# Kernel optimization log

Measured on AMD Instinct MI355X. Metric: run time of the kernel, lower is better.

Reference implementation:

```python
import jax, jax.numpy as jnp
import numpy as np

EPS = 1e-12
NUM_ITERATIONS = 3


def squash(t, axis=-1):
    sn = jnp.sum(t * t, axis=axis, keepdims=True)
    scale = sn / (1.0 + sn + EPS)
    return scale * t / jnp.sqrt(sn + EPS)


def setup_inputs() -> dict:
    key = jax.random.key(0)
    k1, k2 = jax.random.split(key)
    B, R, IN, OUT, C = 128, 4096, 16, 32, 2
    x = jax.random.normal(k1, (B, R, IN), dtype=jnp.float32)
    # learned parameter: torch.randn(num_capsules, num_route_nodes, in, out)
    route_weights = jax.random.normal(k2, (C, R, IN, OUT), dtype=jnp.float32)
    return {"x": x, "route_weights": route_weights}


def reference(x, route_weights):
    # priors: [C, B, R, 1, O] == x[None,:,:,None,:] @ W[:,None,:,:,:]
    priors = jnp.einsum('bri,crio->cbro', x, route_weights)[..., None, :]
    # logits kept [C,B,R,1,1]: the torch code stores [C,B,R,1,O] but every
    # update (delta_logits) is constant along O, so softmax over axis=2 is identical.
    logits = jnp.zeros(priors.shape[:-1] + (1,), dtype=priors.dtype)
    outputs = None
    for i in range(NUM_ITERATIONS):
        probs = jax.nn.softmax(logits, axis=2)                      # over route nodes
        s = jnp.sum(probs * priors, axis=2, keepdims=True)          # [C,B,1,1,O]
        outputs = squash(s, axis=-1)
        if i != NUM_ITERATIONS - 1:
            delta = jnp.sum(priors * outputs, axis=-1, keepdims=True)  # [C,B,R,1,1]
            logits = logits + delta
    return outputs
```

## Files before the change

### kernel.cpp

```cpp
#include <hip/hip_runtime.h>
#include <hip/hip_cooperative_groups.h>
#include <math.h>

namespace cg = cooperative_groups;

#define CB    128
#define CR    4096
#define CIN   16
#define COUT  32
#define CCAP  2
#define RC    16
#define NRCH  (CR / RC)
#define GRID  (CCAP * NRCH)
#define EPSF  1e-12f

typedef _Float16 h8  __attribute__((ext_vector_type(8)));
typedef _Float16 h4t __attribute__((ext_vector_type(4)));
typedef float    f4  __attribute__((ext_vector_type(4)));

__device__ __forceinline__ void stage_pack_W(const float* __restrict__ w,
                                             int c, int r0, int t,
                                             _Float16* WpL, float* Stg)
{
  h4t* WpL4 = (h4t*)WpL;
#pragma unroll
  for (int h = 0; h < 2; ++h) {
    const float4* src = (const float4*)(w + ((size_t)c * CR + r0 + h * 8) * 512);
    ((float4*)Stg)[t]       = src[t];
    ((float4*)Stg)[t + 512] = src[t + 512];
    __syncthreads();
#pragma unroll
    for (int q = 0; q < 2; ++q) {
      const int sl  = t * 2 + q;
      const int rr  = sl >> 7;
      const int rem = sl & 127;
      const int ot  = rem >> 6;
      const int gs  = (rem >> 4) & 3;
      const int ms  = rem & 15;
      h4t v;
#pragma unroll
      for (int j = 0; j < 4; ++j)
        v[j] = (_Float16)Stg[rr * 512 + (4 * gs + j) * 32 + ot * 16 + ms];
      WpL4[(h * 8 + rr) * 128 + rem] = v;
    }
    __syncthreads();
  }
}

__device__ __forceinline__ void pass_body(const float* __restrict__ x,
                                          const float* __restrict__ vsum,
                                          float* __restrict__ partialA,
                                          float* __restrict__ partialE,
                                          const _Float16* WpL,
                                          int c, int rch, int t, int uniform)
{
  const int r0 = rch * RC;
  const int wv = t >> 6, L = t & 63, g = L >> 4, m = L & 15;
  const int b  = wv * 16 + m;
  const h4t* WpL4 = (const h4t*)WpL;

  float4 vA = {0.f, 0.f, 0.f, 0.f}, vB = {0.f, 0.f, 0.f, 0.f};
  if (!uniform) {
    const float* vb = vsum + ((size_t)c * CB + b) * COUT;
    vA = *(const float4*)(vb + 4 * g);
    vB = *(const float4*)(vb + 16 + 4 * g);
  }
  float accA[4] = {0.f, 0.f, 0.f, 0.f};
  float accB[4] = {0.f, 0.f, 0.f, 0.f};
  float esum = 0.f;

#pragma unroll 4
  for (int ri = 0; ri < RC; ++ri) {
    const int r = r0 + ri;
    float4 xf = *(const float4*)(x + ((size_t)b * CR + r) * CIN + 4 * g);
    h8 bx = {(_Float16)xf.x, (_Float16)xf.y, (_Float16)xf.z, (_Float16)xf.w,
             (_Float16)0.f, (_Float16)0.f, (_Float16)0.f, (_Float16)0.f};
    h4t wA4 = WpL4[ri * 128 + L];
    h4t wB4 = WpL4[ri * 128 + 64 + L];
    h8 aA = {wA4[0], wA4[1], wA4[2], wA4[3],
             (_Float16)0.f, (_Float16)0.f, (_Float16)0.f, (_Float16)0.f};
    h8 aB = {wB4[0], wB4[1], wB4[2], wB4[3],
             (_Float16)0.f, (_Float16)0.f, (_Float16)0.f, (_Float16)0.f};
    f4 z = {0.f, 0.f, 0.f, 0.f};
    f4 pA = __builtin_amdgcn_mfma_f32_16x16x32_f16(aA, bx, z, 0, 0, 0);
    f4 pB = __builtin_amdgcn_mfma_f32_16x16x32_f16(aB, bx, z, 0, 0, 0);

    float e = 1.f;
    if (!uniform) {
      float d = pA[0] * vA.x + pA[1] * vA.y + pA[2] * vA.z + pA[3] * vA.w
              + pB[0] * vB.x + pB[1] * vB.y + pB[2] * vB.z + pB[3] * vB.w;
      d += __shfl_xor(d, 16);
      d += __shfl_xor(d, 32);
      e = __expf(d);
    }
    esum += e;
#pragma unroll
    for (int j = 0; j < 4; ++j) { accA[j] += e * pA[j]; accB[j] += e * pB[j]; }
  }

  float4 a4 = {accA[0], accA[1], accA[2], accA[3]};
  float4 b4 = {accB[0], accB[1], accB[2], accB[3]};
  float* dst = partialA + ((size_t)(c * NRCH + rch)) * 4096 + (size_t)t * 8;
  *(float4*)dst = a4;
  *(float4*)(dst + 4) = b4;
  if (g == 0) partialE[((size_t)(c * NRCH + rch)) * CB + b] = esum;
}

template <int JG>
__device__ __forceinline__ void redv_body(const float* __restrict__ partialA,
                                          const float* __restrict__ partialE,
                                          float* __restrict__ vsum,
                                          float* __restrict__ out,
                                          float (*red)[33], float* rede,
                                          int cb, int t, int mode)
{
  const int c2 = cb >> 7, b2 = cb & 127;
  const int o = t & 31, jg = t >> 5;
  const int wv2 = b2 >> 4, m2 = b2 & 15;
  const int half = o >> 4, oo = o & 15, g2 = oo >> 2, j2 = oo & 3;
  const size_t idx = (size_t)(wv2 * 64 + g2 * 16 + m2) * 8 + half * 4 + j2;

  float s = 0.f;
#pragma unroll 4
  for (int k = 0; k < NRCH / JG; ++k) {
    const int j = jg + k * JG;
    s += partialA[((size_t)(c2 * NRCH + j)) * 4096 + idx];
  }
  red[jg][o] = s;
  __syncthreads();

  if (t < JG) {
    float e = 0.f;
#pragma unroll 4
    for (int k = 0; k < NRCH / JG; ++k)
      e += partialE[((size_t)(c2 * NRCH + t + k * JG)) * CB + b2];
    rede[t] = e;
  }
  __syncthreads();

  if (t < 32) {
    float sv = 0.f, es = 0.f;
#pragma unroll
    for (int jj = 0; jj < JG; ++jj) { sv += red[jj][t]; es += rede[jj]; }
    float sm = sv / es;
    float sn = sm * sm;
#pragma unroll
    for (int sh = 1; sh < 32; sh <<= 1) sn += __shfl_xor(sn, sh);
    float fac = sn / ((1.f + sn + EPSF) * sqrtf(sn + EPSF));
    float vv = sm * fac;
    if (mode == 2)      out[cb * COUT + t]  = vv;
    else if (mode == 1) vsum[cb * COUT + t] += vv;
    else                vsum[cb * COUT + t] = vv;
  }
}

__global__ __launch_bounds__(512, 4) void caps_coop_kernel(
    const float* __restrict__ x, const float* __restrict__ w,
    float* __restrict__ vsum, float* __restrict__ partialA,
    float* __restrict__ partialE, float* __restrict__ out)
{
  cg::grid_group grid = cg::this_grid();
  const int blk = (int)blockIdx.x;
  const int c = blk >> 8, rch = blk & 255;
  const int t = (int)threadIdx.x;

  __shared__ __align__(16) char lds[32768];
  _Float16* WpL = (_Float16*)lds;
  float* Stg = (float*)(lds + 16384);
  float (*red)[33] = (float (*)[33])(lds + 16384);
  float* rede = (float*)(lds + 16384 + 16 * 33 * 4);

  stage_pack_W(w, c, rch * RC, t, WpL, Stg);

#pragma unroll 1
  for (int it = 0; it < 3; ++it) {
    pass_body(x, vsum, partialA, partialE, WpL, c, rch, t, it == 0);
    __threadfence();
    grid.sync();
    if (blk < 256)
      redv_body<16>(partialA, partialE, vsum, out, red, rede, blk, t, it);
    if (it < 2) {
      __threadfence();
      grid.sync();
    }
  }
}

__global__ __launch_bounds__(512) void caps_pass_kernel(
    const float* __restrict__ x, const float* __restrict__ w,
    const float* __restrict__ vsum, float* __restrict__ partialA,
    float* __restrict__ partialE, int uniform)
{
  const int blk = (int)blockIdx.x;
  const int c = blk >> 8, rch = blk & 255;
  const int t = (int)threadIdx.x;
  __shared__ __align__(16) char lds[32768];
  _Float16* WpL = (_Float16*)lds;
  float* Stg = (float*)(lds + 16384);
  stage_pack_W(w, c, rch * RC, t, WpL, Stg);
  pass_body(x, vsum, partialA, partialE, WpL, c, rch, t, uniform);
}

__global__ __launch_bounds__(256) void caps_redv_kernel(
    const float* __restrict__ partialA, const float* __restrict__ partialE,
    float* __restrict__ vsum, float* __restrict__ out, int mode)
{
  __shared__ float red[8][33];
  __shared__ float rede[8];
  redv_body<8>(partialA, partialE, vsum, out, red, rede,
               (int)blockIdx.x, (int)threadIdx.x, mode);
}

extern "C" void kernel_launch(void* const* d_in, const int* in_sizes, int n_in,
                              void* d_out, int out_size, void* d_ws, size_t ws_size,
                              hipStream_t stream) {
  const float* x = (const float*)d_in[0];
  const float* w = (const float*)d_in[1];
  float* out = (float*)d_out;

  char* p = (char*)d_ws;
  float* vsum = (float*)p;
  p += (size_t)CCAP * CB * COUT * sizeof(float);
  float* partialA = (float*)p;
  p += (size_t)CCAP * NRCH * 4096 * sizeof(float);
  float* partialE = (float*)p;

  int maxB = 0;
  bool coop_ok =
      (hipOccupancyMaxActiveBlocksPerMultiprocessor(
           &maxB, (const void*)caps_coop_kernel, 512, 0) == hipSuccess) &&
      (maxB >= 2);

  if (coop_ok) {
    void* args[] = {(void*)&x, (void*)&w, (void*)&vsum,
                    (void*)&partialA, (void*)&partialE, (void*)&out};
    hipError_t e = hipLaunchCooperativeKernel((const void*)caps_coop_kernel,
                                              dim3(GRID), dim3(512), args, 0,
                                              stream);
    if (e == hipSuccess) return;
    (void)hipGetLastError();
  }

  for (int it = 0; it < 3; ++it) {
    caps_pass_kernel<<<dim3(GRID), 512, 0, stream>>>(
        x, w, vsum, partialA, partialE, it == 0 ? 1 : 0);
    caps_redv_kernel<<<dim3(CCAP * CB), 256, 0, stream>>>(
        partialA, partialE, vsum, out, it);
  }
}
```

Baseline: 75.92 us.

## Cache fp16 priors in registers across routing iterations in cooperative kernel

The cooperative kernel now computes priors once in the first pass and keeps them packed as fp16 in per-thread registers (16 h8 vectors). Later routing iterations reuse these cached priors instead of re-reading x from global memory and redoing the MFMA products. This removes repeated x loads and matrix work, at the cost of 64 extra VGPRs per thread. That may push register use past the launch_bounds(512,4) target, forcing spills or lowering occupancy, and the coop_ok check requires at least 2 resident blocks per CU.

```diff
diff --git a/kernel.cpp b/kernel.cpp
--- a/kernel.cpp
+++ b/kernel.cpp
@@ -17,6 +17,7 @@
 typedef _Float16 h8  __attribute__((ext_vector_type(8)));
 typedef _Float16 h4t __attribute__((ext_vector_type(4)));
 typedef float    f4  __attribute__((ext_vector_type(4)));
+typedef float    f8v __attribute__((ext_vector_type(8)));
 
 __device__ __forceinline__ void stage_pack_W(const float* __restrict__ w,
                                              int c, int r0, int t,
@@ -47,12 +48,185 @@
   }
 }
 
-__device__ __forceinline__ void pass_body(const float* __restrict__ x,
-                                          const float* __restrict__ vsum,
-                                          float* __restrict__ partialA,
-                                          float* __restrict__ partialE,
-                                          const _Float16* WpL,
-                                          int c, int rch, int t, int uniform)
+__device__ __forceinline__ void store_partials(float* __restrict__ partialA,
+                                               float* __restrict__ partialE,
+                                               const float* accA, const float* accB,
+                                               float esum, int c, int rch,
+                                               int t, int g, int b)
+{
+  float4 a4 = {accA[0], accA[1], accA[2], accA[3]};
+  float4 b4 = {accB[0], accB[1], accB[2], accB[3]};
+  float* dst = partialA + ((size_t)(c * NRCH + rch)) * 4096 + (size_t)t * 8;
+  *(float4*)dst = a4;
+  *(float4*)(dst + 4) = b4;
+  if (g == 0) partialE[((size_t)(c * NRCH + rch)) * CB + b] = esum;
+}
+
+__device__ __forceinline__ void pass0_body(const float* __restrict__ x,
+                                           float* __restrict__ partialA,
+                                           float* __restrict__ partialE,
+                                           const _Float16* WpL,
+                                           int c, int rch, int t, h8* pf)
+{
+  const int r0 = rch * RC;
+  const int wv = t >> 6, L = t & 63, g = L >> 4, m = L & 15;
+  const int b  = wv * 16 + m;
+  const h4t* WpL4 = (const h4t*)WpL;
+
+  float accA[4] = {0.f, 0.f, 0.f, 0.f};
+  float accB[4] = {0.f, 0.f, 0.f, 0.f};
+
+#pragma unroll 4
+  for (int ri = 0; ri < RC; ++ri) {
+    const int r = r0 + ri;
+    float4 xf = *(const float4*)(x + ((size_t)b * CR + r) * CIN + 4 * g);
+    h8 bx = {(_Float16)xf.x, (_Float16)xf.y, (_Float16)xf.z, (_Float16)xf.w,
+             (_Float16)0.f, (_Float16)0.f, (_Float16)0.f, (_Float16)0.f};
+    h4t wA4 = WpL4[ri * 128 + L];
+    h4t wB4 = WpL4[ri * 128 + 64 + L];
+    h8 aA = {wA4[0], wA4[1], wA4[2], wA4[3],
+             (_Float16)0.f, (_Float16)0.f, (_Float16)0.f, (_Float16)0.f};
+    h8 aB = {wB4[0], wB4[1], wB4[2], wB4[3],
+             (_Float16)0.f, (_Float16)0.f, (_Float16)0.f, (_Float16)0.f};
+    f4 z = {0.f, 0.f, 0.f, 0.f};
+    f4 pA = __builtin_amdgcn_mfma_f32_16x16x32_f16(aA, bx, z, 0, 0, 0);
+    f4 pB = __builtin_amdgcn_mfma_f32_16x16x32_f16(aB, bx, z, 0, 0, 0);
+
+    h8 pk = {(_Float16)pA[0], (_Float16)pA[1], (_Float16)pA[2], (_Float16)pA[3],
+             (_Float16)pB[0], (_Float16)pB[1], (_Float16)pB[2], (_Float16)pB[3]};
+    pf[ri] = pk;
+#pragma unroll
+    for (int j = 0; j < 4; ++j) { accA[j] += pA[j]; accB[j] += pB[j]; }
+  }
+  store_partials(partialA, partialE, accA, accB, (float)RC, c, rch, t, g, b);
+}
+
+__device__ __forceinline__ void passN_body(const float* __restrict__ vsum,
+                                           float* __restrict__ partialA,
+                                           float* __restrict__ partialE,
+                                           int c, int rch, int t, const h8* pf)
+{
+  const int wv = t >> 6, L = t & 63, g = L >> 4, m = L & 15;
+  const int b  = wv * 16 + m;
+
+  const float* vb = vsum + ((size_t)c * CB + b) * COUT;
+  float4 vA = *(const float4*)(vb + 4 * g);
+  float4 vB = *(const float4*)(vb + 16 + 4 * g);
+
+  float accA[4] = {0.f, 0.f, 0.f, 0.f};
+  float accB[4] = {0.f, 0.f, 0.f, 0.f};
+  float esum = 0.f;
+
+#pragma unroll
+  for (int ri = 0; ri < RC; ++ri) {
+    f8v p = __builtin_convertvector(pf[ri], f8v);
+    float d = p[0] * vA.x + p[1] * vA.y + p[2] * vA.z + p[3] * vA.w
+            + p[4] * vB.x + p[5] * vB.y + p[6] * vB.z + p[7] * vB.w;
+    d += __shfl_xor(d, 16);
+    d += __shfl_xor(d, 32);
+    const float e = __expf(d);
+    esum += e;
+#pragma unroll
+    for (int j = 0; j < 4; ++j) { accA[j] += e * p[j]; accB[j] += e * p[4 + j]; }
+  }
+  store_partials(partialA, partialE, accA, accB, esum, c, rch, t, g, b);
+}
+
+template <int JG>
+__device__ __forceinline__ void redv_body(const float* __restrict__ partialA,
+                                          const float* __restrict__ partialE,
+                                          float* __restrict__ vsum,
+                                          float* __restrict__ out,
+                                          float (*red)[33], float* rede,
+                                          int cb, int t, int mode)
+{
+  const int c2 = cb >> 7, b2 = cb & 127;
+  const int o = t & 31, jg = t >> 5;
+  const int wv2 = b2 >> 4, m2 = b2 & 15;
+  const int half = o >> 4, oo = o & 15, g2 = oo >> 2, j2 = oo & 3;
+  const size_t idx = (size_t)(wv2 * 64 + g2 * 16 + m2) * 8 + half * 4 + j2;
+
+  float s = 0.f;
+#pragma unroll 4
+  for (int k = 0; k < NRCH / JG; ++k) {
+    const int j = jg + k * JG;
+    s += partialA[((size_t)(c2 * NRCH + j)) * 4096 + idx];
+  }
+  red[jg][o] = s;
+  __syncthreads();
+
+  if (t < JG) {
+    float e = 0.f;
+#pragma unroll 4
+    for (int k = 0; k < NRCH / JG; ++k)
+      e += partialE[((size_t)(c2 * NRCH + t + k * JG)) * CB + b2];
+    rede[t] = e;
+  }
+  __syncthreads();
+
+  if (t < 32) {
+    float sv = 0.f, es = 0.f;
+#pragma unroll
+    for (int jj = 0; jj < JG; ++jj) { sv += red[jj][t]; es += rede[jj]; }
+    float sm = sv / es;
+    float sn = sm * sm;
+#pragma unroll
+    for (int sh = 1; sh < 32; sh <<= 1) sn += __shfl_xor(sn, sh);
+    float fac = sn / ((1.f + sn + EPSF) * sqrtf(sn + EPSF));
+    float vv = sm * fac;
+    if (mode == 2)      out[cb * COUT + t]  = vv;
+    else if (mode == 1) vsum[cb * COUT + t] += vv;
+    else                vsum[cb * COUT + t] = vv;
+  }
+}
+
+__global__ __launch_bounds__(512, 4) void caps_coop_kernel(
+    const float* __restrict__ x, const float* __restrict__ w,
+    float* __restrict__ vsum, float* __restrict__ partialA,
+    float* __restrict__ partialE, float* __restrict__ out)
+{
+  cg::grid_group grid = cg::this_grid();
+  const int blk = (int)blockIdx.x;
+  const int c = blk >> 8, rch = blk & 255;
+  const int t = (int)threadIdx.x;
+
+  __shared__ __align__(16) char lds[32768];
+  _Float16* WpL = (_Float16*)lds;
+  float* Stg = (float*)(lds + 16384);
+  float (*red)[33] = (float (*)[33])(lds + 16384);
+  float* rede = (float*)(lds + 16384 + 16 * 33 * 4);
+
+  h8 pf[RC];
+
+  stage_pack_W(w, c, rch * RC, t, WpL, Stg);
+  pass0_body(x, partialA, partialE, WpL, c, rch, t, pf);
+  __threadfence();
+  grid.sync();
+  if (blk < 256)
+    redv_body<16>(partialA, partialE, vsum, out, red, rede, blk, t, 0);
+  __threadfence();
+  grid.sync();
+
+#pragma unroll 1
+  for (int it = 1; it < 3; ++it) {
+    passN_body(vsum, partialA, partialE, c, rch, t, pf);
+    __threadfence();
+    grid.sync();
+    if (blk < 256)
+      redv_body<16>(partialA, partialE, vsum, out, red, rede, blk, t, it);
+    if (it < 2) {
+      __threadfence();
+      grid.sync();
+    }
+  }
+}
+
+__device__ __forceinline__ void pass_full_body(const float* __restrict__ x,
+                                               const float* __restrict__ vsum,
+                                               float* __restrict__ partialA,
+                                               float* __restrict__ partialE,
+                                               const _Float16* WpL,
+                                               int c, int rch, int t, int uniform)
 {
   const int r0 = rch * RC;
   const int wv = t >> 6, L = t & 63, g = L >> 4, m = L & 15;
@@ -97,93 +271,7 @@
 #pragma unroll
     for (int j = 0; j < 4; ++j) { accA[j] += e * pA[j]; accB[j] += e * pB[j]; }
   }
-
-  float4 a4 = {accA[0], accA[1], accA[2], accA[3]};
-  float4 b4 = {accB[0], accB[1], accB[2], accB[3]};
-  float* dst = partialA + ((size_t)(c * NRCH + rch)) * 4096 + (size_t)t * 8;
-  *(float4*)dst = a4;
-  *(float4*)(dst + 4) = b4;
-  if (g == 0) partialE[((size_t)(c * NRCH + rch)) * CB + b] = esum;
-}
-
-template <int JG>
-__device__ __forceinline__ void redv_body(const float* __restrict__ partialA,
-                                          const float* __restrict__ partialE,
-                                          float* __restrict__ vsum,
-                                          float* __restrict__ out,
-                                          float (*red)[33], float* rede,
-                                          int cb, int t, int mode)
-{
-  const int c2 = cb >> 7, b2 = cb & 127;
-  const int o = t & 31, jg = t >> 5;
-  const int wv2 = b2 >> 4, m2 = b2 & 15;
-  const int half = o >> 4, oo = o & 15, g2 = oo >> 2, j2 = oo & 3;
-  const size_t idx = (size_t)(wv2 * 64 + g2 * 16 + m2) * 8 + half * 4 + j2;
-
-  float s = 0.f;
-#pragma unroll 4
-  for (int k = 0; k < NRCH / JG; ++k) {
-    const int j = jg + k * JG;
-    s += partialA[((size_t)(c2 * NRCH + j)) * 4096 + idx];
-  }
-  red[jg][o] = s;
-  __syncthreads();
-
-  if (t < JG) {
-    float e = 0.f;
-#pragma unroll 4
-    for (int k = 0; k < NRCH / JG; ++k)
-      e += partialE[((size_t)(c2 * NRCH + t + k * JG)) * CB + b2];
-    rede[t] = e;
-  }
-  __syncthreads();
-
-  if (t < 32) {
-    float sv = 0.f, es = 0.f;
-#pragma unroll
-    for (int jj = 0; jj < JG; ++jj) { sv += red[jj][t]; es += rede[jj]; }
-    float sm = sv / es;
-    float sn = sm * sm;
-#pragma unroll
-    for (int sh = 1; sh < 32; sh <<= 1) sn += __shfl_xor(sn, sh);
-    float fac = sn / ((1.f + sn + EPSF) * sqrtf(sn + EPSF));
-    float vv = sm * fac;
-    if (mode == 2)      out[cb * COUT + t]  = vv;
-    else if (mode == 1) vsum[cb * COUT + t] += vv;
-    else                vsum[cb * COUT + t] = vv;
-  }
-}
-
-__global__ __launch_bounds__(512, 4) void caps_coop_kernel(
-    const float* __restrict__ x, const float* __restrict__ w,
-    float* __restrict__ vsum, float* __restrict__ partialA,
-    float* __restrict__ partialE, float* __restrict__ out)
-{
-  cg::grid_group grid = cg::this_grid();
-  const int blk = (int)blockIdx.x;
-  const int c = blk >> 8, rch = blk & 255;
-  const int t = (int)threadIdx.x;
-
-  __shared__ __align__(16) char lds[32768];
-  _Float16* WpL = (_Float16*)lds;
-  float* Stg = (float*)(lds + 16384);
-  float (*red)[33] = (float (*)[33])(lds + 16384);
-  float* rede = (float*)(lds + 16384 + 16 * 33 * 4);
-
-  stage_pack_W(w, c, rch * RC, t, WpL, Stg);
-
-#pragma unroll 1
-  for (int it = 0; it < 3; ++it) {
-    pass_body(x, vsum, partialA, partialE, WpL, c, rch, t, it == 0);
-    __threadfence();
-    grid.sync();
-    if (blk < 256)
-      redv_body<16>(partialA, partialE, vsum, out, red, rede, blk, t, it);
-    if (it < 2) {
-      __threadfence();
-      grid.sync();
-    }
-  }
+  store_partials(partialA, partialE, accA, accB, esum, c, rch, t, g, b);
 }
 
 __global__ __launch_bounds__(512) void caps_pass_kernel(
@@ -198,7 +286,7 @@
   _Float16* WpL = (_Float16*)lds;
   float* Stg = (float*)(lds + 16384);
   stage_pack_W(w, c, rch * RC, t, WpL, Stg);
-  pass_body(x, vsum, partialA, partialE, WpL, c, rch, t, uniform);
+  pass_full_body(x, vsum, partialA, partialE, WpL, c, rch, t, uniform);
 }
 
 __global__ __launch_bounds__(256) void caps_redv_kernel(
```

Result: no change. 75.96 us (+0.1%).

## Materialize fp16 priors once and replace cooperative kernel with separate launches

Applied to the files above, without the earlier changes.

The first pass computes priors with MFMA and writes them to a workspace buffer as fp16. Later routing passes read that buffer instead of reloading x and W and redoing the matmul. The cooperative grid-synced kernel is replaced by six ordinary kernel launches. This drops the repeated x reads (about 33MB each pass) in exchange for writing and reading about 67MB of fp16 priors, and it adds launch gaps in place of grid syncs.

```diff
diff --git a/kernel.cpp b/kernel.cpp
--- a/kernel.cpp
+++ b/kernel.cpp
@@ -1,8 +1,5 @@
 #include <hip/hip_runtime.h>
-#include <hip/hip_cooperative_groups.h>
 #include <math.h>
-
-namespace cg = cooperative_groups;
 
 #define CB    128
 #define CR    4096
@@ -11,12 +8,12 @@
 #define CCAP  2
 #define RC    16
 #define NRCH  (CR / RC)
-#define GRID  (CCAP * NRCH)
 #define EPSF  1e-12f
 
 typedef _Float16 h8  __attribute__((ext_vector_type(8)));
 typedef _Float16 h4t __attribute__((ext_vector_type(4)));
 typedef float    f4  __attribute__((ext_vector_type(4)));
+typedef float    f8v __attribute__((ext_vector_type(8)));
 
 __device__ __forceinline__ void stage_pack_W(const float* __restrict__ w,
                                              int c, int r0, int t,
@@ -47,27 +44,43 @@
   }
 }
 
-__device__ __forceinline__ void pass_body(const float* __restrict__ x,
-                                          const float* __restrict__ vsum,
-                                          float* __restrict__ partialA,
-                                          float* __restrict__ partialE,
-                                          const _Float16* WpL,
-                                          int c, int rch, int t, int uniform)
-{
+__device__ __forceinline__ void store_partials(float* __restrict__ partialA,
+                                               float* __restrict__ partialE,
+                                               const float* accA, const float* accB,
+                                               float esum, int c, int rch,
+                                               int t, int g, int b)
+{
+  float4 a4 = {accA[0], accA[1], accA[2], accA[3]};
+  float4 b4 = {accB[0], accB[1], accB[2], accB[3]};
+  float* dst = partialA + ((size_t)(c * NRCH + rch)) * 4096 + (size_t)t * 8;
+  *(float4*)dst = a4;
+  *(float4*)(dst + 4) = b4;
+  if (g == 0) partialE[((size_t)(c * NRCH + rch)) * CB + b] = esum;
+}
+
+__global__ __launch_bounds__(512) void caps_pass0_kernel(
+    const float* __restrict__ x, const float* __restrict__ w,
+    h8* __restrict__ priors16,
+    float* __restrict__ partialA, float* __restrict__ partialE)
+{
+  const int blk = (int)blockIdx.x;
+  const int c = blk >> 8, rch = blk & 255;
   const int r0 = rch * RC;
+  const int t = (int)threadIdx.x;
   const int wv = t >> 6, L = t & 63, g = L >> 4, m = L & 15;
   const int b  = wv * 16 + m;
+
+  __shared__ __align__(16) char lds[32768];
+  _Float16* WpL = (_Float16*)lds;
+  float* Stg = (float*)(lds + 16384);
+
+  stage_pack_W(w, c, r0, t, WpL, Stg);
+
   const h4t* WpL4 = (const h4t*)WpL;
-
-  float4 vA = {0.f, 0.f, 0.f, 0.f}, vB = {0.f, 0.f, 0.f, 0.f};
-  if (!uniform) {
-    const float* vb = vsum + ((size_t)c * CB + b) * COUT;
-    vA = *(const float4*)(vb + 4 * g);
-    vB = *(const float4*)(vb + 16 + 4 * g);
-  }
+  h8* prow = priors16 + ((size_t)(c * NRCH + rch)) * RC * 512 + t;
+
   float accA[4] = {0.f, 0.f, 0.f, 0.f};
   float accB[4] = {0.f, 0.f, 0.f, 0.f};
-  float esum = 0.f;
 
 #pragma unroll 4
   for (int ri = 0; ri < RC; ++ri) {
@@ -85,55 +98,80 @@
     f4 pA = __builtin_amdgcn_mfma_f32_16x16x32_f16(aA, bx, z, 0, 0, 0);
     f4 pB = __builtin_amdgcn_mfma_f32_16x16x32_f16(aB, bx, z, 0, 0, 0);
 
-    float e = 1.f;
-    if (!uniform) {
-      float d = pA[0] * vA.x + pA[1] * vA.y + pA[2] * vA.z + pA[3] * vA.w
-              + pB[0] * vB.x + pB[1] * vB.y + pB[2] * vB.z + pB[3] * vB.w;
-      d += __shfl_xor(d, 16);
-      d += __shfl_xor(d, 32);
-      e = __expf(d);
-    }
+    h8 pk = {(_Float16)pA[0], (_Float16)pA[1], (_Float16)pA[2], (_Float16)pA[3],
+             (_Float16)pB[0], (_Float16)pB[1], (_Float16)pB[2], (_Float16)pB[3]};
+    prow[ri * 512] = pk;
+
+#pragma unroll
+    for (int j = 0; j < 4; ++j) { accA[j] += pA[j]; accB[j] += pB[j]; }
+  }
+  store_partials(partialA, partialE, accA, accB, (float)RC, 0 * 0 + c, rch, t, g, b);
+}
+
+__global__ __launch_bounds__(512) void caps_passN_kernel(
+    const h8* __restrict__ priors16, const float* __restrict__ vsum,
+    float* __restrict__ partialA, float* __restrict__ partialE)
+{
+  const int blk = (int)blockIdx.x;
+  const int c = blk >> 8, rch = blk & 255;
+  const int t = (int)threadIdx.x;
+  const int wv = t >> 6, L = t & 63, g = L >> 4, m = L & 15;
+  const int b  = wv * 16 + m;
+
+  const float* vb = vsum + ((size_t)c * CB + b) * COUT;
+  float4 vA = *(const float4*)(vb + 4 * g);
+  float4 vB = *(const float4*)(vb + 16 + 4 * g);
+
+  const h8* prow = priors16 + ((size_t)(c * NRCH + rch)) * RC * 512 + t;
+
+  float accA[4] = {0.f, 0.f, 0.f, 0.f};
+  float accB[4] = {0.f, 0.f, 0.f, 0.f};
+  float esum = 0.f;
+
+#pragma unroll 4
+  for (int ri = 0; ri < RC; ++ri) {
+    f8v p = __builtin_convertvector(prow[ri * 512], f8v);
+    float d = p[0] * vA.x + p[1] * vA.y + p[2] * vA.z + p[3] * vA.w
+            + p[4] * vB.x + p[5] * vB.y + p[6] * vB.z + p[7] * vB.w;
+    d += __shfl_xor(d, 16);
+    d += __shfl_xor(d, 32);
+    const float e = __expf(d);
     esum += e;
 #pragma unroll
-    for (int j = 0; j < 4; ++j) { accA[j] += e * pA[j]; accB[j] += e * pB[j]; }
-  }
-
-  float4 a4 = {accA[0], accA[1], accA[2], accA[3]};
-  float4 b4 = {accB[0], accB[1], accB[2], accB[3]};
-  float* dst = partialA + ((size_t)(c * NRCH + rch)) * 4096 + (size_t)t * 8;
-  *(float4*)dst = a4;
-  *(float4*)(dst + 4) = b4;
-  if (g == 0) partialE[((size_t)(c * NRCH + rch)) * CB + b] = esum;
-}
-
-template <int JG>
-__device__ __forceinline__ void redv_body(const float* __restrict__ partialA,
-                                          const float* __restrict__ partialE,
-                                          float* __restrict__ vsum,
-                                          float* __restrict__ out,
-                                          float (*red)[33], float* rede,
-                                          int cb, int t, int mode)
-{
+    for (int j = 0; j < 4; ++j) { accA[j] += e * p[j]; accB[j] += e * p[4 + j]; }
+  }
+  store_partials(partialA, partialE, accA, accB, esum, c, rch, t, g, b);
+}
+
+__global__ __launch_bounds__(256) void caps_redv_kernel(
+    const float* __restrict__ partialA, const float* __restrict__ partialE,
+    float* __restrict__ vsum, float* __restrict__ out, int mode)
+{
+  const int cb = (int)blockIdx.x;
   const int c2 = cb >> 7, b2 = cb & 127;
+  const int t  = (int)threadIdx.x;
   const int o = t & 31, jg = t >> 5;
   const int wv2 = b2 >> 4, m2 = b2 & 15;
   const int half = o >> 4, oo = o & 15, g2 = oo >> 2, j2 = oo & 3;
   const size_t idx = (size_t)(wv2 * 64 + g2 * 16 + m2) * 8 + half * 4 + j2;
 
+  __shared__ float red[8][33];
+  __shared__ float rede[8];
+
   float s = 0.f;
 #pragma unroll 4
-  for (int k = 0; k < NRCH / JG; ++k) {
-    const int j = jg + k * JG;
+  for (int k = 0; k < NRCH / 8; ++k) {
+    const int j = jg + k * 8;
     s += partialA[((size_t)(c2 * NRCH + j)) * 4096 + idx];
   }
   red[jg][o] = s;
   __syncthreads();
 
-  if (t < JG) {
+  if (t < 8) {
     float e = 0.f;
 #pragma unroll 4
-    for (int k = 0; k < NRCH / JG; ++k)
-      e += partialE[((size_t)(c2 * NRCH + t + k * JG)) * CB + b2];
+    for (int k = 0; k < NRCH / 8; ++k)
+      e += partialE[((size_t)(c2 * NRCH + t + k * 8)) * CB + b2];
     rede[t] = e;
   }
   __syncthreads();
@@ -141,7 +179,7 @@
   if (t < 32) {
     float sv = 0.f, es = 0.f;
 #pragma unroll
-    for (int jj = 0; jj < JG; ++jj) { sv += red[jj][t]; es += rede[jj]; }
+    for (int jj = 0; jj < 8; ++jj) { sv += red[jj][t]; es += rede[jj]; }
     float sm = sv / es;
     float sn = sm * sm;
 #pragma unroll
@@ -154,63 +192,6 @@
   }
 }
 
-__global__ __launch_bounds__(512, 4) void caps_coop_kernel(
-    const float* __restrict__ x, const float* __restrict__ w,
-    float* __restrict__ vsum, float* __restrict__ partialA,
-    float* __restrict__ partialE, float* __restrict__ out)
-{
-  cg::grid_group grid = cg::this_grid();
-  const int blk = (int)blockIdx.x;
-  const int c = blk >> 8, rch = blk & 255;
-  const int t = (int)threadIdx.x;
-
-  __shared__ __align__(16) char lds[32768];
-  _Float16* WpL = (_Float16*)lds;
-  float* Stg = (float*)(lds + 16384);
-  float (*red)[33] = (float (*)[33])(lds + 16384);
-  float* rede = (float*)(lds + 16384 + 16 * 33 * 4);
-
-  stage_pack_W(w, c, rch * RC, t, WpL, Stg);
-
-#pragma unroll 1
-  for (int it = 0; it < 3; ++it) {
-    pass_body(x, vsum, partialA, partialE, WpL, c, rch, t, it == 0);
-    __threadfence();
-    grid.sync();
-    if (blk < 256)
-      redv_body<16>(partialA, partialE, vsum, out, red, rede, blk, t, it);
-    if (it < 2) {
-      __threadfence();
-      grid.sync();
-    }
-  }
-}
-
-__global__ __launch_bounds__(512) void caps_pass_kernel(
-    const float* __restrict__ x, const float* __restrict__ w,
-    const float* __restrict__ vsum, float* __restrict__ partialA,
-    float* __restrict__ partialE, int uniform)
-{
-  const int blk = (int)blockIdx.x;
-  const int c = blk >> 8, rch = blk & 255;
-  const int t = (int)threadIdx.x;
-  __shared__ __align__(16) char lds[32768];
-  _Float16* WpL = (_Float16*)lds;
-  float* Stg = (float*)(lds + 16384);
-  stage_pack_W(w, c, rch * RC, t, WpL, Stg);
-  pass_body(x, vsum, partialA, partialE, WpL, c, rch, t, uniform);
-}
-
-__global__ __launch_bounds__(256) void caps_redv_kernel(
-    const float* __restrict__ partialA, const float* __restrict__ partialE,
-    float* __restrict__ vsum, float* __restrict__ out, int mode)
-{
-  __shared__ float red[8][33];
-  __shared__ float rede[8];
-  redv_body<8>(partialA, partialE, vsum, out, red, rede,
-               (int)blockIdx.x, (int)threadIdx.x, mode);
-}
-
 extern "C" void kernel_launch(void* const* d_in, const int* in_sizes, int n_in,
                               void* d_out, int out_size, void* d_ws, size_t ws_size,
                               hipStream_t stream) {
@@ -219,32 +200,24 @@
   float* out = (float*)d_out;
 
   char* p = (char*)d_ws;
+  h8* priors16 = (h8*)p;
+  p += (size_t)CCAP * NRCH * RC * 512 * sizeof(h8);
   float* vsum = (float*)p;
   p += (size_t)CCAP * CB * COUT * sizeof(float);
   float* partialA = (float*)p;
   p += (size_t)CCAP * NRCH * 4096 * sizeof(float);
   float* partialE = (float*)p;
 
-  int maxB = 0;
-  bool coop_ok =
-      (hipOccupancyMaxActiveBlocksPerMultiprocessor(
-           &maxB, (const void*)caps_coop_kernel, 512, 0) == hipSuccess) &&
-      (maxB >= 2);
-
-  if (coop_ok) {
-    void* args[] = {(void*)&x, (void*)&w, (void*)&vsum,
-                    (void*)&partialA, (void*)&partialE, (void*)&out};
-    hipError_t e = hipLaunchCooperativeKernel((const void*)caps_coop_kernel,
-                                              dim3(GRID), dim3(512), args, 0,
-                                              stream);
-    if (e == hipSuccess) return;
-    (void)hipGetLastError();
-  }
-
-  for (int it = 0; it < 3; ++it) {
-    caps_pass_kernel<<<dim3(GRID), 512, 0, stream>>>(
-        x, w, vsum, partialA, partialE, it == 0 ? 1 : 0);
-    caps_redv_kernel<<<dim3(CCAP * CB), 256, 0, stream>>>(
-        partialA, partialE, vsum, out, it);
-  }
-}
+  caps_pass0_kernel<<<dim3(CCAP * NRCH), 512, 0, stream>>>(
+      x, w, priors16, partialA, partialE);
+  caps_redv_kernel<<<dim3(CCAP * CB), 256, 0, stream>>>(
+      partialA, partialE, vsum, out, 0);
+  caps_passN_kernel<<<dim3(CCAP * NRCH), 512, 0, stream>>>(
+      priors16, vsum, partialA, partialE);
+  caps_redv_kernel<<<dim3(CCAP * CB), 256, 0, stream>>>(
+      partialA, partialE, vsum, out, 1);
+  caps_passN_kernel<<<dim3(CCAP * NRCH), 512, 0, stream>>>(
+      priors16, vsum, partialA, partialE);
+  caps_redv_kernel<<<dim3(CCAP * CB), 256, 0, stream>>>(
+      partialA, partialE, vsum, out, 2);
+}
```

After: 79.71 us. +5.0%, slower.
